# Kernel tuning notes

Measured on AMD Instinct MI355X. Metric: run time of the kernel, lower is better.

Reference implementation:

```python
import jax, jax.numpy as jnp
import numpy as np

N_HEADS = 16
NEG_INF = -1e9


def _apply_rope(xq, xk, cos, sin):
    # xq, xk: [B, S, H, hd]; cos/sin: [S, hd//2]
    def rot(t):
        B, S, H, hd = t.shape
        t = t.reshape(B, S, H, hd // 2, 2)
        t0, t1 = t[..., 0], t[..., 1]
        c = cos[None, :, None, :]
        s = sin[None, :, None, :]
        o0 = t0 * c - t1 * s
        o1 = t0 * s + t1 * c
        return jnp.stack([o0, o1], axis=-1).reshape(B, S, H, hd)
    return rot(xq), rot(xk)


def setup_inputs() -> dict:
    key = jax.random.key(0)
    ks = jax.random.split(key, 7)
    B, S, D = 2, 2048, 2048
    hd = D // N_HEADS
    return {
        "x": jax.random.normal(ks[0], (B, S, D), dtype=jnp.float32),
        "freqs_cos": jax.random.uniform(ks[1], (S, hd // 2), dtype=jnp.float32),
        "freqs_sin": jax.random.uniform(ks[2], (S, hd // 2), dtype=jnp.float32),
        "wq": jax.random.normal(ks[3], (D, D), dtype=jnp.float32) * 0.02,
        "wk": jax.random.normal(ks[4], (D, D), dtype=jnp.float32) * 0.02,
        "wv": jax.random.normal(ks[5], (D, D), dtype=jnp.float32) * 0.02,
        "wo": jax.random.normal(ks[6], (D, D), dtype=jnp.float32) * 0.02,
    }


def reference(x, freqs_cos, freqs_sin, wq, wk, wv, wo):
    B, S, D = x.shape
    H = N_HEADS
    hd = D // H

    # projections (torch Linear: y = x @ W.T)
    xq = (x @ wq.T).reshape(B, S, H, hd)
    xk = (x @ wk.T).reshape(B, S, H, hd)
    xv = (x @ wv.T).reshape(B, S, H, hd)

    xq, xk = _apply_rope(xq, xk, freqs_cos, freqs_sin)

    # [B, H, S, hd]
    q = xq.transpose(0, 2, 1, 3)
    k = xk.transpose(0, 2, 1, 3)
    v = xv.transpose(0, 2, 1, 3)

    scores = jnp.einsum("bhqd,bhkd->bhqk", q, k) / jnp.sqrt(jnp.float32(hd))
    causal = jnp.triu(jnp.full((S, S), NEG_INF, dtype=scores.dtype), k=1)
    scores = scores + causal[None, None]
    probs = jax.nn.softmax(scores.astype(jnp.float32), axis=-1).astype(q.dtype)

    out = jnp.einsum("bhqk,bhkd->bhqd", probs, v)
    out = out.transpose(0, 2, 1, 3).reshape(B, S, D)
    return out @ wo.T
```

## Files before the change

kernel.cpp:

```cpp
#include <hip/hip_runtime.h>
#include <hip/hip_bf16.h>
#include <math.h>

typedef __attribute__((ext_vector_type(8))) short short8;
typedef __attribute__((ext_vector_type(4))) short short4v;
typedef __attribute__((ext_vector_type(4))) float f32x4;
typedef unsigned short ushort_t;

__device__ __forceinline__ ushort_t f2bf(float f) {
    union { float f; unsigned u; } v; v.f = f;
    unsigned r = v.u + 0x7FFF + ((v.u >> 16) & 1);
    return (ushort_t)(r >> 16);
}

__global__ void cvt_all(const float* __restrict__ x,
                        const float* __restrict__ w0, const float* __restrict__ w1,
                        const float* __restrict__ w2, const float* __restrict__ w3,
                        const float* __restrict__ fc, const float* __restrict__ fs,
                        ushort_t* __restrict__ dst, float2* __restrict__ fcs,
                        int md8, int dd8, int npair4) {
    int i = blockIdx.x * blockDim.x + threadIdx.x;
    int stride = gridDim.x * blockDim.x;
    const int total0 = md8 + 4 * dd8;
    const int total = total0 + npair4;
    for (; i < total; i += stride) {
        if (i < total0) {
            const float* src;
            long off;
            if (i < md8) { src = x; off = i; }
            else {
                int j = i - md8;
                int which = j / dd8;
                off = j - (long)which * dd8;
                src = (which == 0) ? w0 : (which == 1) ? w1 : (which == 2) ? w2 : w3;
            }
            const float4* s = reinterpret_cast<const float4*>(src) + off * 2;
            float4 a = s[0], b = s[1];
            short8 o;
            o[0] = (short)f2bf(a.x); o[1] = (short)f2bf(a.y);
            o[2] = (short)f2bf(a.z); o[3] = (short)f2bf(a.w);
            o[4] = (short)f2bf(b.x); o[5] = (short)f2bf(b.y);
            o[6] = (short)f2bf(b.z); o[7] = (short)f2bf(b.w);
            reinterpret_cast<short8*>(dst)[i] = o;
        } else {
            int j = i - total0;
            float4 c4 = reinterpret_cast<const float4*>(fc)[j];
            float4 s4 = reinterpret_cast<const float4*>(fs)[j];
            float2* o = fcs + (long)j * 4;
            o[0] = make_float2(c4.x, s4.x);
            o[1] = make_float2(c4.y, s4.y);
            o[2] = make_float2(c4.z, s4.z);
            o[3] = make_float2(c4.w, s4.w);
        }
    }
}

__global__ __launch_bounds__(512, 2) void gemm256_qkv(const ushort_t* __restrict__ A,
                                                      const ushort_t* __restrict__ Bw,
                                                      ushort_t* __restrict__ Cout,
                                                      ushort_t* __restrict__ Vt,
                                                      const float2* __restrict__ fcs,
                                                      int M, int N, int K) {
    extern __shared__ __align__(16) ushort_t lds[];
    ushort_t* As = lds;
    ushort_t* Bs = lds + 32768;
    const int t = threadIdx.x;
    const int wid = t >> 6, lane = t & 63;
    const int wr = wid >> 2, wc = wid & 3;
    const int lr = lane & 15, lg = lane >> 4;

    const int ntc = N >> 8;
    const int nwg = (M >> 8) * ntc;
    const int bid = blockIdx.y * gridDim.x + blockIdx.x;
    const int cpx = nwg >> 3;
    const int swz = (bid & 7) * cpx + (bid >> 3);
    const int m0 = (swz / ntc) * 256, n0 = (swz % ntc) * 256;

    f32x4 acc[8][4] = {};

    const int r0 = t >> 3;
    const int c0 = (t & 7) ^ (r0 & 7);
    const ushort_t* gA = A + (long)(m0 + r0) * K + c0 * 8;
    const ushort_t* gB = Bw + (long)(n0 + r0) * K + c0 * 8;

    int aoffE[2];
    aoffE[0] = lr * 64 + (((0 + lg) ^ (lr & 7)) << 3);
    aoffE[1] = lr * 64 + (((4 + lg) ^ (lr & 7)) << 3);

    const int nt = K >> 6;

#define STAGE_A(X, h) do { const int p_ = (X) & 1;                                             \
    __builtin_amdgcn_global_load_lds((const __attribute__((address_space(1))) unsigned int*)   \
        (gA + (long)((h) * 128) * K + (X) * 64),                                               \
        (__attribute__((address_space(3))) unsigned int*)(As + (p_ * 2 + (h)) * 8192 + t * 8), \
        16, 0, 0);                                                                             \
    __builtin_amdgcn_global_load_lds((const __attribute__((address_space(1))) unsigned int*)   \
        (gA + (long)((h) * 128 + 64) * K + (X) * 64),                                          \
        (__attribute__((address_space(3))) unsigned int*)(As + (p_ * 2 + (h)) * 8192 + 4096 + t * 8), \
        16, 0, 0); } while (0)

#define STAGE_B(X, h) do { const int p_ = (X) & 1;                                             \
    __builtin_amdgcn_global_load_lds((const __attribute__((address_space(1))) unsigned int*)   \
        (gB + (long)((h) * 128) * K + (X) * 64),                                               \
        (__attribute__((address_space(3))) unsigned int*)(Bs + (p_ * 2 + (h)) * 8192 + t * 8), \
        16, 0, 0);                                                                             \
    __builtin_amdgcn_global_load_lds((const __attribute__((address_space(1))) unsigned int*)   \
        (gB + (long)((h) * 128 + 64) * K + (X) * 64),                                          \
        (__attribute__((address_space(3))) unsigned int*)(Bs + (p_ * 2 + (h)) * 8192 + 4096 + t * 8), \
        16, 0, 0); } while (0)

#define MIDSYNC() do {                                             \
    asm volatile("" ::: "memory");                                 \
    __builtin_amdgcn_s_barrier();                                  \
    asm volatile("s_waitcnt lgkmcnt(0)" ::: "memory");             \
    __builtin_amdgcn_sched_barrier(0); } while (0)

#define ENDBAR() do {                                              \
    asm volatile("" ::: "memory");                                 \
    __builtin_amdgcn_s_barrier(); } while (0)

#define MFMA_Q(AROW, BCOL, AR, BR) do {                            \
    __builtin_amdgcn_s_setprio(1);                                 \
    _Pragma("unroll")                                              \
    for (int ks = 0; ks < 2; ++ks)                                 \
        _Pragma("unroll")                                          \
        for (int m = 0; m < 4; ++m)                                \
            _Pragma("unroll")                                      \
            for (int n = 0; n < 2; ++n)                            \
                acc[(AROW) + m][(BCOL) + n] =                      \
                    __builtin_amdgcn_mfma_f32_16x16x32_bf16((AR)[m][ks], (BR)[n][ks], acc[(AROW) + m][(BCOL) + n], 0, 0, 0); \
    __builtin_amdgcn_s_setprio(0); } while (0)

#define KTILE(U, BUF) do {                                                                     \
    const int Asb = ((BUF) * 2 + wr) * 8192;                                                   \
    const int Bcb = ((BUF) * 2 + (wc >> 1)) * 8192 + (wc & 1) * 4096;                          \
    _Pragma("unroll")                                                                          \
    for (int m = 0; m < 4; ++m)                                                                \
        _Pragma("unroll")                                                                      \
        for (int ks = 0; ks < 2; ++ks)                                                         \
            ar[m][ks] = *reinterpret_cast<const short8*>(&As[Asb + m * 1024 + aoffE[ks]]);     \
    _Pragma("unroll")                                                                          \
    for (int n = 0; n < 2; ++n)                                                                \
        _Pragma("unroll")                                                                      \
        for (int ks = 0; ks < 2; ++ks)                                                         \
            br0[n][ks] = *reinterpret_cast<const short8*>(&Bs[Bcb + n * 1024 + aoffE[ks]]);    \
    if ((U) + 1 < nt) STAGE_A((U) + 1, 1);                                                     \
    MIDSYNC();                                                                                 \
    MFMA_Q(0, 0, ar, br0);                                                                     \
    ENDBAR();                                                                                  \
    _Pragma("unroll")                                                                          \
    for (int n = 0; n < 2; ++n)                                                                \
        _Pragma("unroll")                                                                      \
        for (int ks = 0; ks < 2; ++ks)                                                         \
            br1[n][ks] = *reinterpret_cast<const short8*>(&Bs[Bcb + 2048 + n * 1024 + aoffE[ks]]); \
    MIDSYNC();                                                                                 \
    MFMA_Q(0, 2, ar, br1);                                                                     \
    ENDBAR();                                                                                  \
    _Pragma("unroll")                                                                          \
    for (int m = 0; m < 4; ++m)                                                                \
        _Pragma("unroll")                                                                      \
        for (int ks = 0; ks < 2; ++ks)                                                         \
            ar[m][ks] = *reinterpret_cast<const short8*>(&As[Asb + 4096 + m * 1024 + aoffE[ks]]); \
    if ((U) + 2 < nt) STAGE_B((U) + 2, 0);                                                     \
    MIDSYNC();                                                                                 \
    MFMA_Q(4, 2, ar, br1);                                                                     \
    ENDBAR();                                                                                  \
    if ((U) + 2 < nt) { STAGE_A((U) + 2, 0); STAGE_B((U) + 2, 1); }                            \
    asm volatile("" ::: "memory");                                                             \
    __builtin_amdgcn_s_barrier();                                                              \
    MFMA_Q(4, 0, ar, br0);                                                                     \
    if ((U) < nt - 2) {                                                                        \
        asm volatile("s_waitcnt vmcnt(6)" ::: "memory");                                       \
    } else if ((U) == nt - 2) {                                                                \
        asm volatile("s_waitcnt vmcnt(0)" ::: "memory");                                       \
    }                                                                                          \
    __builtin_amdgcn_s_barrier(); } while (0)

    STAGE_A(0, 0); STAGE_A(0, 1); STAGE_B(0, 0); STAGE_B(0, 1);
    STAGE_A(1, 0); STAGE_B(1, 0); STAGE_B(1, 1);
    asm volatile("s_waitcnt vmcnt(6)" ::: "memory");
    __builtin_amdgcn_s_barrier();

    short8 ar[4][2], br0[2][2], br1[2][2];

    for (int U = 0; U < nt; U += 2) {
        KTILE(U, 0);
        KTILE(U + 1, 1);
    }
#undef KTILE
#undef MFMA_Q
#undef ENDBAR
#undef MIDSYNC
#undef STAGE_A
#undef STAGE_B

    const int S = 2048;
    #pragma unroll
    for (int m = 0; m < 8; ++m) {
        #pragma unroll
        for (int n = 0; n < 4; ++n) {
            const int col = n0 + wc * 64 + n * 16 + lr;
            const int which = col >> 11;
            const int h = (col >> 7) & 15;
            const int d = col & 127;
            const int rowb = m0 + wr * 128 + m * 16 + lg * 4;
            const int bb = rowb >> 11;
            const int sb = rowb & 2047;
            if (which == 2) {
                short4v o;
                #pragma unroll
                for (int r = 0; r < 4; ++r) o[r] = (short)f2bf(acc[m][n][r]);
                *reinterpret_cast<short4v*>(Vt + ((long)(bb * 16 + h) * 128 + d) * S + sb) = o;
            } else {
                const int i0 = d >> 1;
                #pragma unroll
                for (int r = 0; r < 4; ++r) {
                    const int s = sb + r;
                    float v = acc[m][n][r];
                    float p = __shfl_xor(v, 1);
                    float2 cs = fcs[(long)s * 64 + i0];
                    float o = (lr & 1) ? (p * cs.y + v * cs.x) : (v * cs.x - p * cs.y);
                    Cout[(long)which * M * 2048 + (((long)(bb * 16 + h)) * 2048 + s) * 128 + d] = f2bf(o);
                }
            }
        }
    }
}

__global__ __launch_bounds__(256) void gemm_nt_f32(const ushort_t* __restrict__ A,
                                                   const ushort_t* __restrict__ Bw,
                                                   float* __restrict__ Cout,
                                                   int M, int N, int K) {
    __shared__ __align__(16) ushort_t As[2 * 128 * 32];
    __shared__ __align__(16) ushort_t Bs[2 * 128 * 32];
    const int t = threadIdx.x;
    const int wid = t >> 6, lane = t & 63;
    const int wm = wid >> 1, wn = wid & 1;
    const int lr = lane & 15, lg = lane >> 4;

    const int ntc = N >> 7;
    const int nwg = (M >> 7) * ntc;
    const int bid = blockIdx.y * gridDim.x + blockIdx.x;
    const int cpx = nwg >> 3;
    const int swz = (bid & 7) * cpx + (bid >> 3);
    const int m0 = (swz / ntc) * 128, n0 = (swz % ntc) * 128;

    f32x4 acc[4][4] = {};

    const int sh0 = wid * 1024 + lane * 8;
    const int sh1 = sh0 + 512;
    const int r0 = sh0 >> 5, c0 = sh0 & 31;
    const int r1 = sh1 >> 5, c1 = sh1 & 31;

    const ushort_t* gA0 = A + (long)(m0 + r0) * K + c0;
    const ushort_t* gA1 = A + (long)(m0 + r1) * K + c1;
    const ushort_t* gB0 = Bw + (long)(n0 + r0) * K + c0;
    const ushort_t* gB1 = Bw + (long)(n0 + r1) * K + c1;

    auto stage = [&](int k0, int nb) {
        ushort_t* as = As + nb * 4096;
        ushort_t* bs = Bs + nb * 4096;
        __builtin_amdgcn_global_load_lds((const __attribute__((address_space(1))) unsigned int*)(gA0 + k0),
                                         (__attribute__((address_space(3))) unsigned int*)(as + sh0), 16, 0, 0);
        __builtin_amdgcn_global_load_lds((const __attribute__((address_space(1))) unsigned int*)(gA1 + k0),
                                         (__attribute__((address_space(3))) unsigned int*)(as + sh1), 16, 0, 0);
        __builtin_amdgcn_global_load_lds((const __attribute__((address_space(1))) unsigned int*)(gB0 + k0),
                                         (__attribute__((address_space(3))) unsigned int*)(bs + sh0), 16, 0, 0);
        __builtin_amdgcn_global_load_lds((const __attribute__((address_space(1))) unsigned int*)(gB1 + k0),
                                         (__attribute__((address_space(3))) unsigned int*)(bs + sh1), 16, 0, 0);
    };

    const int nt = K >> 5;
    stage(0, 0);
    __syncthreads();
    int cur = 0;

    for (int ti = 0; ti < nt; ++ti) {
        if (ti + 1 < nt) stage((ti + 1) << 5, cur ^ 1);
        const ushort_t* as = As + cur * 4096;
        const ushort_t* bs = Bs + cur * 4096;
        short8 af[4], bfr[4];
        #pragma unroll
        for (int m = 0; m < 4; ++m)
            af[m] = *reinterpret_cast<const short8*>(&as[(wm * 64 + m * 16 + lr) * 32 + lg * 8]);
        #pragma unroll
        for (int n = 0; n < 4; ++n)
            bfr[n] = *reinterpret_cast<const short8*>(&bs[(wn * 64 + n * 16 + lr) * 32 + lg * 8]);
        #pragma unroll
        for (int m = 0; m < 4; ++m)
            #pragma unroll
            for (int n = 0; n < 4; ++n)
                acc[m][n] = __builtin_amdgcn_mfma_f32_16x16x32_bf16(af[m], bfr[n], acc[m][n], 0, 0, 0);
        __syncthreads();
        cur ^= 1;
    }

    #pragma unroll
    for (int m = 0; m < 4; ++m) {
        #pragma unroll
        for (int n = 0; n < 4; ++n) {
            const int col = n0 + wn * 64 + n * 16 + lr;
            #pragma unroll
            for (int r = 0; r < 4; ++r) {
                const int row = m0 + wm * 64 + m * 16 + lg * 4 + r;
                Cout[(long)row * N + col] = acc[m][n][r];
            }
        }
    }
}

__global__ __launch_bounds__(256, 3) void attn_kernel(const ushort_t* __restrict__ Qp,
                                                      const ushort_t* __restrict__ Kp,
                                                      const ushort_t* __restrict__ Vtg,
                                                      ushort_t* __restrict__ O,
                                                      int S, int H) {
    __shared__ __align__(16) ushort_t Ks[64 * 128];
    __shared__ __align__(16) ushort_t Vs[128 * 64];
    __shared__ __align__(16) ushort_t Pl[4][16][72];
    const int t = threadIdx.x, wid = t >> 6, lane = t & 63;
    const int lr = lane & 15, lg = lane >> 4;
    const int bh = blockIdx.y;
    const int b = bh / H, h = bh % H;
    const ushort_t* Qh = Qp + (long)bh * S * 128;
    const ushort_t* Kh = Kp + (long)bh * S * 128;
    const ushort_t* Vth = Vtg + (long)bh * 128 * S;
    const int nq = S / 64;
    const float scale = 0.08838834764831845f;

    const int ksr = t >> 2;
    const int vsr = t & 127;
    const int vsc = (t >> 7) * 32;

    for (int qsel = 0; qsel < 2; ++qsel) {
        const int qt = qsel ? (nq - 1 - blockIdx.x) : blockIdx.x;
        const int qb0 = qt * 64;

        const int qrow = qb0 + wid * 16 + lr;
        short8 qf[4];
        #pragma unroll
        for (int kk = 0; kk < 4; ++kk)
            qf[kk] = *reinterpret_cast<const short8*>(Qh + (long)qrow * 128 + kk * 32 + lg * 8);

        f32x4 oacc[8] = {};
        float mrow[4], lsum[4];
        #pragma unroll
        for (int r = 0; r < 4; ++r) { mrow[r] = -INFINITY; lsum[r] = 0.f; }

        const int nkt = qt + 1;

        short8 kreg[4], vreg[4];
        {
            const ushort_t* kgp = Kh + t * 32;
            const ushort_t* vgp = Vth + (long)vsr * S + vsc;
            #pragma unroll
            for (int j = 0; j < 4; ++j) kreg[j] = *reinterpret_cast<const short8*>(kgp + j * 8);
            #pragma unroll
            for (int j = 0; j < 4; ++j) vreg[j] = *reinterpret_cast<const short8*>(vgp + j * 8);
        }

        for (int kt = 0; kt < nkt; ++kt) {
            const int kv0 = kt * 64;
            __syncthreads();
            #pragma unroll
            for (int j = 0; j < 4; ++j)
                *reinterpret_cast<short8*>(&Ks[(ksr << 7) + (((((t & 3) << 2) + j) ^ (ksr & 7)) << 3)]) = kreg[j];
            #pragma unroll
            for (int j = 0; j < 4; ++j)
                *reinterpret_cast<short8*>(&Vs[(vsr << 6) + (((((t >> 7) << 2) + j) ^ (vsr & 7)) << 3)]) = vreg[j];
            __syncthreads();
            if (kt + 1 < nkt) {
                const ushort_t* kgp = Kh + (long)(kv0 + 64) * 128 + t * 32;
                const ushort_t* vgp = Vth + (long)vsr * S + kv0 + 64 + vsc;
                #pragma unroll
                for (int j = 0; j < 4; ++j) kreg[j] = *reinterpret_cast<const short8*>(kgp + j * 8);
                #pragma unroll
                for (int j = 0; j < 4; ++j) vreg[j] = *reinterpret_cast<const short8*>(vgp + j * 8);
            }

            f32x4 sacc[4] = {};
            #pragma unroll
            for (int kk = 0; kk < 4; ++kk) {
                #pragma unroll
                for (int n = 0; n < 4; ++n) {
                    short8 kf = *reinterpret_cast<const short8*>(
                        &Ks[((n * 16 + lr) << 7) + ((((kk << 2) + lg) ^ (lr & 7)) << 3)]);
                    sacc[n] = __builtin_amdgcn_mfma_f32_16x16x32_bf16(qf[kk], kf, sacc[n], 0, 0, 0);
                }
            }
            float sv[4][4];
            const int myq = qb0 + wid * 16 + lg * 4;
            #pragma unroll
            for (int n = 0; n < 4; ++n) {
                int kcol = kv0 + n * 16 + lr;
                #pragma unroll
                for (int r = 0; r < 4; ++r) {
                    float xv = sacc[n][r] * scale;
                    sv[n][r] = (kcol > myq + r) ? -1e9f : xv;
                }
            }
            float alpha[4];
            #pragma unroll
            for (int r = 0; r < 4; ++r) {
                float mx = fmaxf(fmaxf(sv[0][r], sv[1][r]), fmaxf(sv[2][r], sv[3][r]));
                #pragma unroll
                for (int off = 1; off < 16; off <<= 1)
                    mx = fmaxf(mx, __shfl_xor(mx, off));
                float mnew = fmaxf(mrow[r], mx);
                alpha[r] = __expf(mrow[r] - mnew);
                float ts = 0.f;
                #pragma unroll
                for (int n = 0; n < 4; ++n) {
                    float p = __expf(sv[n][r] - mnew);
                    sv[n][r] = p;
                    ts += p;
                }
                #pragma unroll
                for (int off = 1; off < 16; off <<= 1)
                    ts += __shfl_xor(ts, off);
                lsum[r] = lsum[r] * alpha[r] + ts;
                mrow[r] = mnew;
            }
            #pragma unroll
            for (int f = 0; f < 8; ++f)
                #pragma unroll
                for (int r = 0; r < 4; ++r)
                    oacc[f][r] *= alpha[r];
            #pragma unroll
            for (int n = 0; n < 4; ++n)
                #pragma unroll
                for (int r = 0; r < 4; ++r)
                    Pl[wid][lg * 4 + r][n * 16 + lr] = f2bf(sv[n][r]);
            __asm volatile("" ::: "memory");
            short8 pf[2];
            #pragma unroll
            for (int ks = 0; ks < 2; ++ks)
                pf[ks] = *reinterpret_cast<const short8*>(&Pl[wid][lr][ks * 32 + lg * 8]);
            #pragma unroll
            for (int ks = 0; ks < 2; ++ks) {
                #pragma unroll
                for (int f = 0; f < 8; ++f) {
                    short8 vf = *reinterpret_cast<const short8*>(
                        &Vs[((f * 16 + lr) << 6) + ((((ks << 2) + lg) ^ (lr & 7)) << 3)]);
                    oacc[f] = __builtin_amdgcn_mfma_f32_16x16x32_bf16(pf[ks], vf, oacc[f], 0, 0, 0);
                }
            }
        }
        float inv[4];
        #pragma unroll
        for (int r = 0; r < 4; ++r) inv[r] = 1.f / lsum[r];
        ushort_t* Oh = O + (long)b * S * 2048 + h * 128;
        #pragma unroll
        for (int f = 0; f < 8; ++f) {
            #pragma unroll
            for (int r = 0; r < 4; ++r) {
                int row = qb0 + wid * 16 + lg * 4 + r;
                int col = f * 16 + lr;
                Oh[(long)row * 2048 + col] = f2bf(oacc[f][r] * inv[r]);
            }
        }
    }
}

extern "C" void kernel_launch(void* const* d_in, const int* in_sizes, int n_in,
                              void* d_out, int out_size, void* d_ws, size_t ws_size,
                              hipStream_t stream) {
    const float* x  = (const float*)d_in[0];
    const float* fc = (const float*)d_in[1];
    const float* fs = (const float*)d_in[2];
    const float* wq = (const float*)d_in[3];
    const float* wk = (const float*)d_in[4];
    const float* wv = (const float*)d_in[5];
    const float* wo = (const float*)d_in[6];
    float* out = (float*)d_out;

    const int B = 2, S = 2048, D = 2048, H = 16;
    const int M = B * S;
    const size_t MD = (size_t)M * D;
    const size_t DD = (size_t)D * D;

    char* ws = (char*)d_ws;
    ushort_t* xbf = (ushort_t*)ws;
    ushort_t* wqb = (ushort_t*)(ws + MD * 2);
    ushort_t* wob = wqb + 3 * DD;
    ushort_t* qp  = wqb + 4 * DD;
    ushort_t* kp  = qp + MD;
    ushort_t* vtg = kp + MD;
    float2* fcs   = (float2*)(vtg + MD);
    ushort_t* attnb = xbf;

    const int npair4 = S * 64 / 4;
    cvt_all<<<2048, 256, 0, stream>>>(x, wq, wk, wv, wo, fc, fs, xbf, fcs,
                                      (int)(MD / 8), (int)(DD / 8), npair4);

    dim3 gq(6144 / 256, M / 256);
    gemm256_qkv<<<gq, 512, 131072, stream>>>(xbf, wqb, qp, vtg, fcs, M, 3 * D, D);

    dim3 ga(S / 128, B * H);
    attn_kernel<<<ga, 256, 0, stream>>>(qp, kp, vtg, attnb, S, H);

    dim3 gg(D / 128, M / 128);
    gemm_nt_f32<<<gg, 256, 0, stream>>>(attnb, wob, out, M, D, D);
}
```

Before: 309.1 us.

## Shrink QKV GEMM tile to 128x256, fold softmax scale into Q, pad P LDS

The QKV projection GEMM tile shrinks from 256x256 to 128x256, which doubles the workgroup count and restructures the LDS staging and the K-loop schedule to match. LDS per block drops from 128KB to 96KB. The softmax scale times log2(e) is now folded into Q in the GEMM epilogue, so attention can use exp2f and skip the per-score multiply. The padding on the P LDS buffer rows also grows from 72 to 80. The smaller tile aims for better occupancy and load balance but lowers the reuse of each B tile.

```diff
diff --git a/kernel.cpp b/kernel.cpp
--- a/kernel.cpp
+++ b/kernel.cpp
@@ -6,6 +6,8 @@
 typedef __attribute__((ext_vector_type(4))) short short4v;
 typedef __attribute__((ext_vector_type(4))) float f32x4;
 typedef unsigned short ushort_t;
+
+#define QK_LOG2E_SCALE 0.1275274059009601f
 
 __device__ __forceinline__ ushort_t f2bf(float f) {
     union { float f; unsigned u; } v; v.f = f;
@@ -63,20 +65,20 @@
                                                       int M, int N, int K) {
     extern __shared__ __align__(16) ushort_t lds[];
     ushort_t* As = lds;
-    ushort_t* Bs = lds + 32768;
+    ushort_t* Bs = lds + 16384;
     const int t = threadIdx.x;
     const int wid = t >> 6, lane = t & 63;
     const int wr = wid >> 2, wc = wid & 3;
     const int lr = lane & 15, lg = lane >> 4;
 
     const int ntc = N >> 8;
-    const int nwg = (M >> 8) * ntc;
+    const int nwg = (M >> 7) * ntc;
     const int bid = blockIdx.y * gridDim.x + blockIdx.x;
     const int cpx = nwg >> 3;
     const int swz = (bid & 7) * cpx + (bid >> 3);
-    const int m0 = (swz / ntc) * 256, n0 = (swz % ntc) * 256;
-
-    f32x4 acc[8][4] = {};
+    const int m0 = (swz / ntc) * 128, n0 = (swz % ntc) * 256;
+
+    f32x4 acc[4][4] = {};
 
     const int r0 = t >> 3;
     const int c0 = (t & 7) ^ (r0 & 7);
@@ -89,25 +91,20 @@
 
     const int nt = K >> 6;
 
-#define STAGE_A(X, h) do { const int p_ = (X) & 1;                                             \
+#define STAGE_A(X) do { const int p_ = (X) & 1;                                                \
     __builtin_amdgcn_global_load_lds((const __attribute__((address_space(1))) unsigned int*)   \
-        (gA + (long)((h) * 128) * K + (X) * 64),                                               \
-        (__attribute__((address_space(3))) unsigned int*)(As + (p_ * 2 + (h)) * 8192 + t * 8), \
-        16, 0, 0);                                                                             \
+        (gA + (X) * 64),                                                                       \
+        (__attribute__((address_space(3))) unsigned int*)(As + p_ * 8192 + t * 8), 16, 0, 0);  \
     __builtin_amdgcn_global_load_lds((const __attribute__((address_space(1))) unsigned int*)   \
-        (gA + (long)((h) * 128 + 64) * K + (X) * 64),                                          \
-        (__attribute__((address_space(3))) unsigned int*)(As + (p_ * 2 + (h)) * 8192 + 4096 + t * 8), \
-        16, 0, 0); } while (0)
-
-#define STAGE_B(X, h) do { const int p_ = (X) & 1;                                             \
-    __builtin_amdgcn_global_load_lds((const __attribute__((address_space(1))) unsigned int*)   \
-        (gB + (long)((h) * 128) * K + (X) * 64),                                               \
-        (__attribute__((address_space(3))) unsigned int*)(Bs + (p_ * 2 + (h)) * 8192 + t * 8), \
-        16, 0, 0);                                                                             \
-    __builtin_amdgcn_global_load_lds((const __attribute__((address_space(1))) unsigned int*)   \
-        (gB + (long)((h) * 128 + 64) * K + (X) * 64),                                          \
-        (__attribute__((address_space(3))) unsigned int*)(Bs + (p_ * 2 + (h)) * 8192 + 4096 + t * 8), \
-        16, 0, 0); } while (0)
+        (gA + (long)64 * K + (X) * 64),                                                        \
+        (__attribute__((address_space(3))) unsigned int*)(As + p_ * 8192 + 4096 + t * 8), 16, 0, 0); } while (0)
+
+#define STAGE_B(X) do { const int p_ = (X) & 1;                                                \
+    _Pragma("unroll")                                                                          \
+    for (int j_ = 0; j_ < 4; ++j_)                                                             \
+        __builtin_amdgcn_global_load_lds((const __attribute__((address_space(1))) unsigned int*) \
+            (gB + (long)(j_ * 64) * K + (X) * 64),                                             \
+            (__attribute__((address_space(3))) unsigned int*)(Bs + p_ * 16384 + j_ * 4096 + t * 8), 16, 0, 0); } while (0)
 
 #define MIDSYNC() do {                                             \
     asm volatile("" ::: "memory");                                 \
@@ -119,7 +116,7 @@
     asm volatile("" ::: "memory");                                 \
     __builtin_amdgcn_s_barrier(); } while (0)
 
-#define MFMA_Q(AROW, BCOL, AR, BR) do {                            \
+#define MFMA_Q(BCOL, BR) do {                                      \
     __builtin_amdgcn_s_setprio(1);                                 \
     _Pragma("unroll")                                              \
     for (int ks = 0; ks < 2; ++ks)                                 \
@@ -127,13 +124,14 @@
         for (int m = 0; m < 4; ++m)                                \
             _Pragma("unroll")                                      \
             for (int n = 0; n < 2; ++n)                            \
-                acc[(AROW) + m][(BCOL) + n] =                      \
-                    __builtin_amdgcn_mfma_f32_16x16x32_bf16((AR)[m][ks], (BR)[n][ks], acc[(AROW) + m][(BCOL) + n], 0, 0, 0); \
+                acc[m][(BCOL) + n] =                               \
+                    __builtin_amdgcn_mfma_f32_16x16x32_bf16(ar[m][ks], (BR)[n][ks], acc[m][(BCOL) + n], 0, 0, 0); \
     __builtin_amdgcn_s_setprio(0); } while (0)
 
 #define KTILE(U, BUF) do {                                                                     \
-    const int Asb = ((BUF) * 2 + wr) * 8192;                                                   \
-    const int Bcb = ((BUF) * 2 + (wc >> 1)) * 8192 + (wc & 1) * 4096;                          \
+    const int Asb = (BUF) * 8192 + wr * 4096;                                                  \
+    const int Bcb = (BUF) * 16384 + wc * 4096;                                                 \
+                                                             \
     _Pragma("unroll")                                                                          \
     for (int m = 0; m < 4; ++m)                                                                \
         _Pragma("unroll")                                                                      \
@@ -144,31 +142,20 @@
         _Pragma("unroll")                                                                      \
         for (int ks = 0; ks < 2; ++ks)                                                         \
             br0[n][ks] = *reinterpret_cast<const short8*>(&Bs[Bcb + n * 1024 + aoffE[ks]]);    \
-    if ((U) + 1 < nt) STAGE_A((U) + 1, 1);                                                     \
     MIDSYNC();                                                                                 \
-    MFMA_Q(0, 0, ar, br0);                                                                     \
+    MFMA_Q(0, br0);                                                                            \
     ENDBAR();                                                                                  \
+                     \
     _Pragma("unroll")                                                                          \
     for (int n = 0; n < 2; ++n)                                                                \
         _Pragma("unroll")                                                                      \
         for (int ks = 0; ks < 2; ++ks)                                                         \
             br1[n][ks] = *reinterpret_cast<const short8*>(&Bs[Bcb + 2048 + n * 1024 + aoffE[ks]]); \
+    if ((U) + 2 < nt) STAGE_A((U) + 2);                                                        \
     MIDSYNC();                                                                                 \
-    MFMA_Q(0, 2, ar, br1);                                                                     \
-    ENDBAR();                                                                                  \
-    _Pragma("unroll")                                                                          \
-    for (int m = 0; m < 4; ++m)                                                                \
-        _Pragma("unroll")                                                                      \
-        for (int ks = 0; ks < 2; ++ks)                                                         \
-            ar[m][ks] = *reinterpret_cast<const short8*>(&As[Asb + 4096 + m * 1024 + aoffE[ks]]); \
-    if ((U) + 2 < nt) STAGE_B((U) + 2, 0);                                                     \
-    MIDSYNC();                                                                                 \
-    MFMA_Q(4, 2, ar, br1);                                                                     \
-    ENDBAR();                                                                                  \
-    if ((U) + 2 < nt) { STAGE_A((U) + 2, 0); STAGE_B((U) + 2, 1); }                            \
+    MFMA_Q(2, br1);                                                                            \
+    if ((U) + 2 < nt) STAGE_B((U) + 2);                                                        \
     asm volatile("" ::: "memory");                                                             \
-    __builtin_amdgcn_s_barrier();                                                              \
-    MFMA_Q(4, 0, ar, br0);                                                                     \
     if ((U) < nt - 2) {                                                                        \
         asm volatile("s_waitcnt vmcnt(6)" ::: "memory");                                       \
     } else if ((U) == nt - 2) {                                                                \
@@ -176,8 +163,7 @@
     }                                                                                          \
     __builtin_amdgcn_s_barrier(); } while (0)
 
-    STAGE_A(0, 0); STAGE_A(0, 1); STAGE_B(0, 0); STAGE_B(0, 1);
-    STAGE_A(1, 0); STAGE_B(1, 0); STAGE_B(1, 1);
+    STAGE_A(0); STAGE_B(0); STAGE_A(1); STAGE_B(1);
     asm volatile("s_waitcnt vmcnt(6)" ::: "memory");
     __builtin_amdgcn_s_barrier();
 
@@ -196,14 +182,14 @@
 
     const int S = 2048;
     #pragma unroll
-    for (int m = 0; m < 8; ++m) {
+    for (int m = 0; m < 4; ++m) {
         #pragma unroll
         for (int n = 0; n < 4; ++n) {
             const int col = n0 + wc * 64 + n * 16 + lr;
             const int which = col >> 11;
             const int h = (col >> 7) & 15;
             const int d = col & 127;
-            const int rowb = m0 + wr * 128 + m * 16 + lg * 4;
+            const int rowb = m0 + wr * 64 + m * 16 + lg * 4;
             const int bb = rowb >> 11;
             const int sb = rowb & 2047;
             if (which == 2) {
@@ -213,6 +199,7 @@
                 *reinterpret_cast<short4v*>(Vt + ((long)(bb * 16 + h) * 128 + d) * S + sb) = o;
             } else {
                 const int i0 = d >> 1;
+                const float qs = (which == 0) ? QK_LOG2E_SCALE : 1.0f;
                 #pragma unroll
                 for (int r = 0; r < 4; ++r) {
                     const int s = sb + r;
@@ -220,7 +207,7 @@
                     float p = __shfl_xor(v, 1);
                     float2 cs = fcs[(long)s * 64 + i0];
                     float o = (lr & 1) ? (p * cs.y + v * cs.x) : (v * cs.x - p * cs.y);
-                    Cout[(long)which * M * 2048 + (((long)(bb * 16 + h)) * 2048 + s) * 128 + d] = f2bf(o);
+                    Cout[(long)which * M * 2048 + (((long)(bb * 16 + h)) * 2048 + s) * 128 + d] = f2bf(o * qs);
                 }
             }
         }
@@ -316,7 +303,7 @@
                                                       int S, int H) {
     __shared__ __align__(16) ushort_t Ks[64 * 128];
     __shared__ __align__(16) ushort_t Vs[128 * 64];
-    __shared__ __align__(16) ushort_t Pl[4][16][72];
+    __shared__ __align__(16) ushort_t Pl[4][16][80];
     const int t = threadIdx.x, wid = t >> 6, lane = t & 63;
     const int lr = lane & 15, lg = lane >> 4;
     const int bh = blockIdx.y;
@@ -325,7 +312,6 @@
     const ushort_t* Kh = Kp + (long)bh * S * 128;
     const ushort_t* Vth = Vtg + (long)bh * 128 * S;
     const int nq = S / 64;
-    const float scale = 0.08838834764831845f;
 
     const int ksr = t >> 2;
     const int vsr = t & 127;
@@ -393,10 +379,8 @@
             for (int n = 0; n < 4; ++n) {
                 int kcol = kv0 + n * 16 + lr;
                 #pragma unroll
-                for (int r = 0; r < 4; ++r) {
-                    float xv = sacc[n][r] * scale;
-                    sv[n][r] = (kcol > myq + r) ? -1e9f : xv;
-                }
+                for (int r = 0; r < 4; ++r)
+                    sv[n][r] = (kcol > myq + r) ? -1e9f : sacc[n][r];
             }
             float alpha[4];
             #pragma unroll
@@ -406,11 +390,11 @@
                 for (int off = 1; off < 16; off <<= 1)
                     mx = fmaxf(mx, __shfl_xor(mx, off));
                 float mnew = fmaxf(mrow[r], mx);
-                alpha[r] = __expf(mrow[r] - mnew);
+                alpha[r] = exp2f(mrow[r] - mnew);
                 float ts = 0.f;
                 #pragma unroll
                 for (int n = 0; n < 4; ++n) {
-                    float p = __expf(sv[n][r] - mnew);
+                    float p = exp2f(sv[n][r] - mnew);
                     sv[n][r] = p;
                     ts += p;
                 }
@@ -492,8 +476,8 @@
     cvt_all<<<2048, 256, 0, stream>>>(x, wq, wk, wv, wo, fc, fs, xbf, fcs,
                                       (int)(MD / 8), (int)(DD / 8), npair4);
 
-    dim3 gq(6144 / 256, M / 256);
-    gemm256_qkv<<<gq, 512, 131072, stream>>>(xbf, wqb, qp, vtg, fcs, M, 3 * D, D);
+    dim3 gq(6144 / 256, M / 128);
+    gemm256_qkv<<<gq, 512, 98304, stream>>>(xbf, wqb, qp, vtg, fcs, M, 3 * D, D);
 
     dim3 ga(S / 128, B * H);
     attn_kernel<<<ga, 256, 0, stream>>>(qp, kp, vtg, attnb, S, H);
```

Result: no change. 309.6 us (+0.2%).
